# Optimization experiments

Measured on AMD Instinct MI355X. Metric: run time of the kernel, lower is better.

The kernel has to match this reference:

```python
import jax, jax.numpy as jnp
import numpy as np

LEVEL = 256
GROUPS = 1
SHIFT = (LEVEL - 1) / 2.0  # symmetric affine shift folded from quant.shift buffer


def qdq(x, clip_val, level=LEVEL, groups=GROUPS, shift=SHIFT):
    """Per-group clip + level quantize-dequantize (what custom_quant.Quant saves/restores).
    clip_val: [groups]. Group split is over equal contiguous chunks of the flattened tensor."""
    shp = x.shape
    xg = x.reshape(groups, -1)
    scale = (2.0 * clip_val) / (level - 1)          # [groups]
    scale = scale.reshape(groups, 1)
    q = jnp.clip(jnp.round(xg / scale + shift), 0.0, level - 1.0)
    return ((q - shift) * scale).reshape(shp)


def setup_inputs() -> dict:
    key = jax.random.key(0)
    k1, k2 = jax.random.split(key)
    # attention-style batched matmul: [B,H,S,Dh] @ [B,H,Dh,S]
    x1 = jax.random.normal(k1, (2, 12, 1024, 64), dtype=jnp.float32)
    x2 = jax.random.normal(k2, (2, 12, 64, 1024), dtype=jnp.float32)
    clip_val1 = 2.0 * jnp.ones((GROUPS,), dtype=jnp.float32)
    clip_val2 = 2.0 * jnp.ones((GROUPS,), dtype=jnp.float32)
    return {"x1": x1, "x2": x2, "clip_val1": clip_val1, "clip_val2": clip_val2}


def reference(x1, x2, clip_val1, clip_val2):
    # Faithful to matmul.forward: the quantized copies are only SAVED for backward;
    # the forward output itself is computed on the full-precision operands.
    # (qdq is exercised in the fwdbwd reference.)
    return jnp.matmul(x1, x2)  # [2,12,1024,1024]
```

## Files before the change

### kernel.cpp

```cpp
#include <hip/hip_runtime.h>
#include <hip/hip_bf16.h>


#define NN 1024

typedef __attribute__((ext_vector_type(4))) float  float4v;
typedef __attribute__((ext_vector_type(8))) short  bf16x8;
typedef __attribute__((ext_vector_type(16))) float floatx16;

__device__ __forceinline__ short f2bs(float f) {
    union { float f; unsigned u; } in;
    in.f = f;
    unsigned u = in.u;
    return (short)((u + 0x7FFFu + ((u >> 16) & 1u)) >> 16);
}


__global__ __launch_bounds__(256) void reformat_AB(const float* __restrict__ A,
                                                   const float* __restrict__ B,
                                                   short* __restrict__ Aw,
                                                   short* __restrict__ Bw) {
    const int bid = blockIdx.x;
    if (bid < 768) {
        int task = bid * 256 + threadIdx.x;
        int bh   = task >> 13;
        int rem  = task & 8191;
        int m    = rem >> 3;
        int kg   = rem & 7;
        const float4v* p = (const float4v*)(A + (size_t)task * 8);
        float4v v0 = __builtin_nontemporal_load(p);
        float4v v1 = __builtin_nontemporal_load(p + 1);
        int ks = kg >> 1, q = kg & 1;
        int mt = m >> 5;
        int lane = (m & 31) + (q << 5);
        size_t dst = ((size_t)((bh * 32 + mt) * 4 + ks)) * 512 + (size_t)lane * 8;
        bf16x8 o;
        o[0] = f2bs(v0.x); o[1] = f2bs(v0.y); o[2] = f2bs(v0.z); o[3] = f2bs(v0.w);
        o[4] = f2bs(v1.x); o[5] = f2bs(v1.y); o[6] = f2bs(v1.z); o[7] = f2bs(v1.w);
        *(bf16x8*)(Aw + dst) = o;
    } else {
        int task = (bid - 768) * 256 + threadIdx.x;
        int kg   = task / 24576;
        int rem  = task - kg * 24576;
        int bh   = rem >> 10;
        int n    = rem & 1023;
        const float* p = B + (size_t)bh * 65536 + (size_t)kg * 8192 + n;
        float v0 = __builtin_nontemporal_load(p + 0 * 1024);
        float v1 = __builtin_nontemporal_load(p + 1 * 1024);
        float v2 = __builtin_nontemporal_load(p + 2 * 1024);
        float v3 = __builtin_nontemporal_load(p + 3 * 1024);
        float v4 = __builtin_nontemporal_load(p + 4 * 1024);
        float v5 = __builtin_nontemporal_load(p + 5 * 1024);
        float v6 = __builtin_nontemporal_load(p + 6 * 1024);
        float v7 = __builtin_nontemporal_load(p + 7 * 1024);
        int ks = kg >> 1, q = kg & 1;
        int nt = n >> 5;
        int lane = (n & 31) + (q << 5);
        size_t dst = ((size_t)((bh * 32 + nt) * 4 + ks)) * 512 + (size_t)lane * 8;
        bf16x8 o;
        o[0] = f2bs(v0); o[1] = f2bs(v1); o[2] = f2bs(v2); o[3] = f2bs(v3);
        o[4] = f2bs(v4); o[5] = f2bs(v5); o[6] = f2bs(v6); o[7] = f2bs(v7);
        *(bf16x8*)(Bw + dst) = o;
    }
}

__global__ __launch_bounds__(256) void bmm_frag(const short* __restrict__ Aw,
                                                const short* __restrict__ Bw,
                                                float* __restrict__ C) {
    const int tid  = threadIdx.x;
    const int lane = tid & 63;
    const int w    = tid >> 6;
    const int bx = blockIdx.x;
    const int by = blockIdx.y;
    const int bh = blockIdx.z;
    const int wm = (w >> 1) * 2;
    const int wn = (w & 1) * 2;

    const short* Ab = Aw + ((size_t)((bh * 32 + by * 4 + wm) * 4)) * 512 + (size_t)lane * 8;
    const short* Bb = Bw + ((size_t)((bh * 32 + bx * 4 + wn) * 4)) * 512 + (size_t)lane * 8;

    floatx16 acc[2][2];
    #pragma unroll
    for (int mi = 0; mi < 2; ++mi)
        #pragma unroll
        for (int ni = 0; ni < 2; ++ni)
            #pragma unroll
            for (int r = 0; r < 16; ++r)
                acc[mi][ni][r] = 0.0f;

    #pragma unroll
    for (int ks = 0; ks < 4; ++ks) {
        bf16x8 a0 = *(const bf16x8*)(Ab + ks * 512);
        bf16x8 a1 = *(const bf16x8*)(Ab + 2048 + ks * 512);
        bf16x8 b0 = *(const bf16x8*)(Bb + ks * 512);
        bf16x8 b1 = *(const bf16x8*)(Bb + 2048 + ks * 512);
        acc[0][0] = __builtin_amdgcn_mfma_f32_32x32x16_bf16(a0, b0, acc[0][0], 0, 0, 0);
        acc[0][1] = __builtin_amdgcn_mfma_f32_32x32x16_bf16(a0, b1, acc[0][1], 0, 0, 0);
        acc[1][0] = __builtin_amdgcn_mfma_f32_32x32x16_bf16(a1, b0, acc[1][0], 0, 0, 0);
        acc[1][1] = __builtin_amdgcn_mfma_f32_32x32x16_bf16(a1, b1, acc[1][1], 0, 0, 0);
    }

    const int nc    = lane & 31;
    const int rbase = (lane >> 5) * 4;
    float* Cb = C + ((size_t)bh << 20)
                  + (size_t)(by * 128 + wm * 32) * NN
                  + bx * 128 + wn * 32 + nc;

    #pragma unroll
    for (int mi = 0; mi < 2; ++mi) {
        #pragma unroll
        for (int ni = 0; ni < 2; ++ni) {
            float* Ct = Cb + (size_t)(mi * 32) * NN + ni * 32;
            #pragma unroll
            for (int r = 0; r < 16; ++r) {
                int row = rbase + (r & 3) + ((r >> 2) * 8);
                __builtin_nontemporal_store(acc[mi][ni][r], Ct + (size_t)row * NN);
            }
        }
    }
}

extern "C" void kernel_launch(void* const* d_in, const int* in_sizes, int n_in,
                              void* d_out, int out_size, void* d_ws, size_t ws_size,
                              hipStream_t stream) {
    const float* x1 = (const float*)d_in[0];
    const float* x2 = (const float*)d_in[1];
    float* out = (float*)d_out;

    short* Aw = (short*)d_ws;
    short* Bw = Aw + 1572864;

    hipLaunchKernelGGL(reformat_AB, dim3(1536), dim3(256), 0, stream, x1, x2, Aw, Bw);
    hipLaunchKernelGGL(bmm_frag, dim3(8, 8, 24), dim3(256), 0, stream, Aw, Bw, out);
}
```

Baseline: 122.2 us.

## Fuse fp32-to-bf16 conversion into the batched matmul kernel, dropping reformat pass

Removes the separate reformat kernel that converted A and B to bf16 in an MFMA-fragment layout in workspace. The matmul kernel now reads fp32 operands straight from the inputs and converts them to bf16 in registers before the MFMAs. This saves one kernel launch and the workspace write/read round trip. In exchange each block rereads operand tiles in fp32, which is twice the bytes of bf16. B is also loaded as strided scalar loads, which may coalesce less well. The output is still dominated by the 96MB fp32 store.

Result: slower. 134.4 us (+10.0%).

```diff
diff --git a/kernel.cpp b/kernel.cpp
--- a/kernel.cpp
+++ b/kernel.cpp
@@ -1,5 +1,4 @@
 #include <hip/hip_runtime.h>
-#include <hip/hip_bf16.h>
 
 
 #define NN 1024
@@ -15,58 +14,9 @@
     return (short)((u + 0x7FFFu + ((u >> 16) & 1u)) >> 16);
 }
 
-
-__global__ __launch_bounds__(256) void reformat_AB(const float* __restrict__ A,
-                                                   const float* __restrict__ B,
-                                                   short* __restrict__ Aw,
-                                                   short* __restrict__ Bw) {
-    const int bid = blockIdx.x;
-    if (bid < 768) {
-        int task = bid * 256 + threadIdx.x;
-        int bh   = task >> 13;
-        int rem  = task & 8191;
-        int m    = rem >> 3;
-        int kg   = rem & 7;
-        const float4v* p = (const float4v*)(A + (size_t)task * 8);
-        float4v v0 = __builtin_nontemporal_load(p);
-        float4v v1 = __builtin_nontemporal_load(p + 1);
-        int ks = kg >> 1, q = kg & 1;
-        int mt = m >> 5;
-        int lane = (m & 31) + (q << 5);
-        size_t dst = ((size_t)((bh * 32 + mt) * 4 + ks)) * 512 + (size_t)lane * 8;
-        bf16x8 o;
-        o[0] = f2bs(v0.x); o[1] = f2bs(v0.y); o[2] = f2bs(v0.z); o[3] = f2bs(v0.w);
-        o[4] = f2bs(v1.x); o[5] = f2bs(v1.y); o[6] = f2bs(v1.z); o[7] = f2bs(v1.w);
-        *(bf16x8*)(Aw + dst) = o;
-    } else {
-        int task = (bid - 768) * 256 + threadIdx.x;
-        int kg   = task / 24576;
-        int rem  = task - kg * 24576;
-        int bh   = rem >> 10;
-        int n    = rem & 1023;
-        const float* p = B + (size_t)bh * 65536 + (size_t)kg * 8192 + n;
-        float v0 = __builtin_nontemporal_load(p + 0 * 1024);
-        float v1 = __builtin_nontemporal_load(p + 1 * 1024);
-        float v2 = __builtin_nontemporal_load(p + 2 * 1024);
-        float v3 = __builtin_nontemporal_load(p + 3 * 1024);
-        float v4 = __builtin_nontemporal_load(p + 4 * 1024);
-        float v5 = __builtin_nontemporal_load(p + 5 * 1024);
-        float v6 = __builtin_nontemporal_load(p + 6 * 1024);
-        float v7 = __builtin_nontemporal_load(p + 7 * 1024);
-        int ks = kg >> 1, q = kg & 1;
-        int nt = n >> 5;
-        int lane = (n & 31) + (q << 5);
-        size_t dst = ((size_t)((bh * 32 + nt) * 4 + ks)) * 512 + (size_t)lane * 8;
-        bf16x8 o;
-        o[0] = f2bs(v0); o[1] = f2bs(v1); o[2] = f2bs(v2); o[3] = f2bs(v3);
-        o[4] = f2bs(v4); o[5] = f2bs(v5); o[6] = f2bs(v6); o[7] = f2bs(v7);
-        *(bf16x8*)(Bw + dst) = o;
-    }
-}
-
-__global__ __launch_bounds__(256) void bmm_frag(const short* __restrict__ Aw,
-                                                const short* __restrict__ Bw,
-                                                float* __restrict__ C) {
+__global__ __launch_bounds__(256, 4) void bmm_fused(const float* __restrict__ A,
+                                                    const float* __restrict__ B,
+                                                    float* __restrict__ C) {
     const int tid  = threadIdx.x;
     const int lane = tid & 63;
     const int w    = tid >> 6;
@@ -75,9 +25,13 @@
     const int bh = blockIdx.z;
     const int wm = (w >> 1) * 2;
     const int wn = (w & 1) * 2;
+    const int l31 = lane & 31;
+    const int q   = lane >> 5;
 
-    const short* Ab = Aw + ((size_t)((bh * 32 + by * 4 + wm) * 4)) * 512 + (size_t)lane * 8;
-    const short* Bb = Bw + ((size_t)((bh * 32 + bx * 4 + wn) * 4)) * 512 + (size_t)lane * 8;
+    const float* Ab = A + ((size_t)bh << 16)
+                        + (size_t)(by * 128 + wm * 32 + l31) * 64 + q * 8;
+    const float* Bb = B + ((size_t)bh << 16)
+                        + (size_t)(q * 8) * NN + (bx * 128 + wn * 32 + l31);
 
     floatx16 acc[2][2];
     #pragma unroll
@@ -90,18 +44,40 @@
 
     #pragma unroll
     for (int ks = 0; ks < 4; ++ks) {
-        bf16x8 a0 = *(const bf16x8*)(Ab + ks * 512);
-        bf16x8 a1 = *(const bf16x8*)(Ab + 2048 + ks * 512);
-        bf16x8 b0 = *(const bf16x8*)(Bb + ks * 512);
-        bf16x8 b1 = *(const bf16x8*)(Bb + 2048 + ks * 512);
+        const float* pa0 = Ab + ks * 16;
+        const float* pa1 = pa0 + 32 * 64;
+        float4v a0lo = *(const float4v*)(pa0);
+        float4v a0hi = *(const float4v*)(pa0 + 4);
+        float4v a1lo = *(const float4v*)(pa1);
+        float4v a1hi = *(const float4v*)(pa1 + 4);
+
+        const float* pb = Bb + (size_t)(ks * 16) * NN;
+        float b0f[8], b1f[8];
+        #pragma unroll
+        for (int j = 0; j < 8; ++j) {
+            b0f[j] = pb[(size_t)j * NN];
+            b1f[j] = pb[(size_t)j * NN + 32];
+        }
+
+        bf16x8 a0, a1, b0, b1;
+        a0[0] = f2bs(a0lo.x); a0[1] = f2bs(a0lo.y); a0[2] = f2bs(a0lo.z); a0[3] = f2bs(a0lo.w);
+        a0[4] = f2bs(a0hi.x); a0[5] = f2bs(a0hi.y); a0[6] = f2bs(a0hi.z); a0[7] = f2bs(a0hi.w);
+        a1[0] = f2bs(a1lo.x); a1[1] = f2bs(a1lo.y); a1[2] = f2bs(a1lo.z); a1[3] = f2bs(a1lo.w);
+        a1[4] = f2bs(a1hi.x); a1[5] = f2bs(a1hi.y); a1[6] = f2bs(a1hi.z); a1[7] = f2bs(a1hi.w);
+        #pragma unroll
+        for (int j = 0; j < 8; ++j) {
+            b0[j] = f2bs(b0f[j]);
+            b1[j] = f2bs(b1f[j]);
+        }
+
         acc[0][0] = __builtin_amdgcn_mfma_f32_32x32x16_bf16(a0, b0, acc[0][0], 0, 0, 0);
         acc[0][1] = __builtin_amdgcn_mfma_f32_32x32x16_bf16(a0, b1, acc[0][1], 0, 0, 0);
         acc[1][0] = __builtin_amdgcn_mfma_f32_32x32x16_bf16(a1, b0, acc[1][0], 0, 0, 0);
         acc[1][1] = __builtin_amdgcn_mfma_f32_32x32x16_bf16(a1, b1, acc[1][1], 0, 0, 0);
     }
 
-    const int nc    = lane & 31;
-    const int rbase = (lane >> 5) * 4;
+    const int nc    = l31;
+    const int rbase = q * 4;
     float* Cb = C + ((size_t)bh << 20)
                   + (size_t)(by * 128 + wm * 32) * NN
                   + bx * 128 + wn * 32 + nc;
@@ -127,9 +103,7 @@
     const float* x2 = (const float*)d_in[1];
     float* out = (float*)d_out;
 
-    short* Aw = (short*)d_ws;
-    short* Bw = Aw + 1572864;
+    (void)d_ws; (void)ws_size;
 
-    hipLaunchKernelGGL(reformat_AB, dim3(1536), dim3(256), 0, stream, x1, x2, Aw, Bw);
-    hipLaunchKernelGGL(bmm_frag, dim3(8, 8, 24), dim3(256), 0, stream, Aw, Bw, out);
+    hipLaunchKernelGGL(bmm_fused, dim3(8, 8, 24), dim3(256), 0, stream, x1, x2, out);
 }
```
